# Optimization experiments

Hardware: AMD Instinct MI355X
Metric: run time of the kernel (lower is better)

The kernel has to match this reference:

```python
import jax, jax.numpy as jnp
import numpy as np

B, T, C, H = 2, 2048, 2048, 16
D = C // H  # 128


def _rope(x, cos, sin):
    # x: (B, T, H, D); cos/sin: (T, D//2) -> complex rotation on consecutive pairs
    xr = x.reshape(x.shape[0], x.shape[1], x.shape[2], D // 2, 2)
    x0, x1 = xr[..., 0], xr[..., 1]
    c = cos[None, :, None, :]
    s = sin[None, :, None, :]
    out = jnp.stack([x0 * c - x1 * s, x0 * s + x1 * c], axis=-1)
    return out.reshape(x.shape)


def setup_inputs() -> dict:
    key = jax.random.key(0)
    k1, k2, k3 = jax.random.split(key, 3)
    x = jax.random.normal(k1, (B, T, C), dtype=jnp.float32)
    w_qkv = jax.random.normal(k2, (3 * C, C), dtype=jnp.float32) * (C ** -0.5)
    w_proj = jax.random.normal(k3, (C, C), dtype=jnp.float32) * (C ** -0.5)
    # standard RoPE frequencies: theta_i = 10000^{-2i/D}
    inv_freq = 1.0 / (10000.0 ** (np.arange(0, D, 2, dtype=np.float32) / D))
    ang = np.outer(np.arange(T, dtype=np.float32), inv_freq)  # (T, D//2)
    freqs_cos = jnp.asarray(np.cos(ang), dtype=jnp.float32)
    freqs_sin = jnp.asarray(np.sin(ang), dtype=jnp.float32)
    return {"x": x, "w_qkv": w_qkv, "w_proj": w_proj,
            "freqs_cos": freqs_cos, "freqs_sin": freqs_sin}


def reference(x, w_qkv, w_proj, freqs_cos, freqs_sin):
    b, t, c = x.shape
    qkv = (x @ w_qkv.T).reshape(b, t, 3, H, D)
    q, k, v = qkv[:, :, 0], qkv[:, :, 1], qkv[:, :, 2]  # (B,T,H,D)
    q = _rope(q, freqs_cos, freqs_sin)
    k = _rope(k, freqs_cos, freqs_sin)
    scale = 1.0 / jnp.sqrt(jnp.float32(D))
    scores = jnp.einsum('bqhd,bkhd->bhqk', q, k) * scale  # (B,H,T,T)
    causal = jnp.tril(jnp.ones((t, t), dtype=bool))
    scores = jnp.where(causal[None, None], scores, jnp.finfo(scores.dtype).min)
    attn = jax.nn.softmax(scores, axis=-1)
    out = jnp.einsum('bhqk,bkhd->bqhd', attn, v).reshape(b, t, c)
    return out @ w_proj.T
```

## Files before the change

kernel.cpp:

```cpp
#include <hip/hip_runtime.h>
#include <hip/hip_bf16.h>

typedef float f32x4 __attribute__((ext_vector_type(4)));
typedef __bf16 bf16x8 __attribute__((ext_vector_type(8)));
typedef __bf16 bf16x4 __attribute__((ext_vector_type(4)));

constexpr int B_ = 2, T_ = 2048, C_ = 2048, H_ = 16, D_ = 128;
constexpr int M_ = B_ * T_;
constexpr int NQKV_ = 3 * C_;

__device__ __forceinline__ void gload_lds16(const void* g, void* l) {
    __builtin_amdgcn_global_load_lds(
        (const __attribute__((address_space(1))) unsigned int*)g,
        (__attribute__((address_space(3))) unsigned int*)l,
        16, 0, 0);
}

__global__ void cvt_kernel(const float* __restrict__ in, __bf16* __restrict__ out, int n4) {
    int i = blockIdx.x * blockDim.x + threadIdx.x;
    int stride = gridDim.x * blockDim.x;
    for (; i < n4; i += stride) {
        float4 v = reinterpret_cast<const float4*>(in)[i];
        bf16x4 o;
        o[0] = (__bf16)v.x; o[1] = (__bf16)v.y; o[2] = (__bf16)v.z; o[3] = (__bf16)v.w;
        reinterpret_cast<bf16x4*>(out)[i] = o;
    }
}

template <typename OutT>
__global__ __launch_bounds__(256, 3) void gemm_bt(
    const __bf16* __restrict__ A, const __bf16* __restrict__ Bm,
    OutT* __restrict__ Cm, int Mdim, int Ndim, int Kdim)
{
    __shared__ __align__(16) __bf16 As[128 * 64];
    __shared__ __align__(16) __bf16 Bs[128 * 64];
    const int tid = threadIdx.x;
    const int wave = tid >> 6, lane = tid & 63;
    const int fr = lane & 15, fq = lane >> 4;
    const int nbx = Ndim >> 7;
    const int bm = (blockIdx.x / nbx) << 7;
    const int bn = (blockIdx.x % nbx) << 7;
    const int wr = (wave >> 1) * 64, wc = (wave & 1) * 64;
    f32x4 acc[4][4] = {};
    const int srow = (wave << 5) + (lane >> 3);
    const int sch = lane & 7;
    const __bf16* Ag = A + (size_t)(bm + srow) * Kdim + sch * 8;
    const __bf16* Bg = Bm + (size_t)(bn + srow) * Kdim + sch * 8;

    for (int k0 = 0; k0 < Kdim; k0 += 64) {
        __syncthreads();
        #pragma unroll
        for (int p = 0; p < 4; ++p) {
            gload_lds16(Ag + (size_t)(8 * p) * Kdim + k0, (char*)As + (wave * 32 + 8 * p) * 128);
            gload_lds16(Bg + (size_t)(8 * p) * Kdim + k0, (char*)Bs + (wave * 32 + 8 * p) * 128);
        }
        __syncthreads();
        #pragma unroll
        for (int s = 0; s < 2; ++s) {
            bf16x8 af[4], bg[4];
            #pragma unroll
            for (int m = 0; m < 4; ++m)
                af[m] = *reinterpret_cast<const bf16x8*>((const char*)As + (wr + m * 16 + fr) * 128 + s * 64 + fq * 16);
            #pragma unroll
            for (int n = 0; n < 4; ++n)
                bg[n] = *reinterpret_cast<const bf16x8*>((const char*)Bs + (wc + n * 16 + fr) * 128 + s * 64 + fq * 16);
            #pragma unroll
            for (int m = 0; m < 4; ++m)
                #pragma unroll
                for (int n = 0; n < 4; ++n)
                    acc[m][n] = __builtin_amdgcn_mfma_f32_16x16x32_bf16(af[m], bg[n], acc[m][n], 0, 0, 0);
        }
    }
    #pragma unroll
    for (int m = 0; m < 4; ++m) {
        #pragma unroll
        for (int n = 0; n < 4; ++n) {
            int row0 = bm + wr + m * 16 + fq * 4;
            int col = bn + wc + n * 16 + fr;
            #pragma unroll
            for (int i = 0; i < 4; ++i)
                Cm[(size_t)(row0 + i) * Ndim + col] = (OutT)acc[m][n][i];
        }
    }
}

__global__ void rope_pack(const __bf16* __restrict__ qkv,
                          const float* __restrict__ fcos, const float* __restrict__ fsin,
                          __bf16* __restrict__ Q, __bf16* __restrict__ K, __bf16* __restrict__ V)
{
    const int row = blockIdx.x;
    const int b = row >> 11, t = row & (T_ - 1);
    const int tid = threadIdx.x;
    const int h = tid >> 4;
    const int jq = tid & 15;
    const float4 c4 = *reinterpret_cast<const float4*>(fcos + t * 64 + jq * 4);
    const float4 s4 = *reinterpret_cast<const float4*>(fsin + t * 64 + jq * 4);
    const float cc[4] = {c4.x, c4.y, c4.z, c4.w};
    const float ss[4] = {s4.x, s4.y, s4.z, s4.w};
    const __bf16* src = qkv + (size_t)row * NQKV_ + h * D_ + jq * 8;
    const size_t doff = ((size_t)(b * H_ + h) * T_ + t) * D_ + jq * 8;
    #pragma unroll
    for (int s = 0; s < 3; ++s) {
        bf16x8 v = *reinterpret_cast<const bf16x8*>(src + s * C_);
        bf16x8 o;
        if (s == 2) {
            o = v;
        } else {
            #pragma unroll
            for (int e = 0; e < 4; ++e) {
                float x0 = (float)v[2 * e], x1 = (float)v[2 * e + 1];
                o[2 * e]     = (__bf16)(x0 * cc[e] - x1 * ss[e]);
                o[2 * e + 1] = (__bf16)(x0 * ss[e] + x1 * cc[e]);
            }
        }
        __bf16* dst = (s == 0) ? Q : ((s == 1) ? K : V);
        *reinterpret_cast<bf16x8*>(dst + doff) = o;
    }
}

__global__ void transpose_v(const __bf16* __restrict__ V, __bf16* __restrict__ Vt) {
    const int bid = blockIdx.x;
    const int per_bh = (T_ / 64) * (D_ / 64);
    const int bh = bid / per_bh;
    const int rem = bid % per_bh;
    const int t0 = (rem / (D_ / 64)) * 64;
    const int d0 = (rem % (D_ / 64)) * 64;
    __shared__ __align__(16) __bf16 tile[64][72];
    const int tid = threadIdx.x;
    #pragma unroll
    for (int pass = 0; pass < 2; ++pass) {
        int r = pass * 32 + (tid >> 3);
        int ch = tid & 7;
        *reinterpret_cast<bf16x8*>(&tile[r][ch * 8]) =
            *reinterpret_cast<const bf16x8*>(V + ((size_t)bh * T_ + t0 + r) * D_ + d0 + ch * 8);
    }
    __syncthreads();
    #pragma unroll
    for (int pass = 0; pass < 2; ++pass) {
        int dr = pass * 32 + (tid >> 3);
        int ch = tid & 7;
        bf16x8 v;
        #pragma unroll
        for (int e = 0; e < 8; ++e) v[e] = tile[ch * 8 + e][dr];
        *reinterpret_cast<bf16x8*>(Vt + ((size_t)bh * D_ + d0 + dr) * T_ + t0 + ch * 8) = v;
    }
}

__global__ __launch_bounds__(256, 2) void attn_fwd(
    const __bf16* __restrict__ Q, const __bf16* __restrict__ K,
    const __bf16* __restrict__ Vt, __bf16* __restrict__ Out)
{
    const int bh = blockIdx.x;
    const int qt = (T_ / 128 - 1) - blockIdx.y;
    const int tid = threadIdx.x;
    const int wave = tid >> 6, lane = tid & 63;
    const int fr = lane & 15, fq = lane >> 4;
    __shared__ __align__(16) __bf16 Ks[64 * 128];
    __shared__ __align__(16) __bf16 Vs[128 * 64];
    __shared__ __align__(16) __bf16 Ps[4][32 * 64];

    const int q0 = qt * 128 + wave * 32;
    bf16x8 qf[2][4];
    #pragma unroll
    for (int m = 0; m < 2; ++m)
        #pragma unroll
        for (int ks = 0; ks < 4; ++ks)
            qf[m][ks] = *reinterpret_cast<const bf16x8*>(
                Q + ((size_t)bh * T_ + q0 + m * 16 + fr) * D_ + ks * 32 + 8 * fq);

    f32x4 oacc[2][8] = {};
    float mrow[2] = {-3.0e38f, -3.0e38f}, lrow[2] = {0.f, 0.f};
    const float scale = 0.08838834764831845f;
    char* pb = (char*)&Ps[wave][0];
    const int qmax = q0 + 31;
    const int ktmax = 2 * qt + 1;
    const int kr = lane >> 4, kch = lane & 15;
    const int vr = lane >> 3, vch = lane & 7;

    for (int kt = 0; kt <= ktmax; ++kt) {
        __syncthreads();
        #pragma unroll
        for (int p = 0; p < 4; ++p) {
            int row = 16 * wave + 4 * p + kr;
            gload_lds16(K + ((size_t)bh * T_ + kt * 64 + row) * D_ + ((kch ^ (row & 7)) << 3),
                        (char*)Ks + (16 * wave + 4 * p) * 256);
        }
        #pragma unroll
        for (int p = 0; p < 4; ++p) {
            int row = 32 * wave + 8 * p + vr;
            gload_lds16(Vt + ((size_t)bh * D_ + row) * T_ + kt * 64 + ((vch ^ (row & 7)) << 3),
                        (char*)Vs + (32 * wave + 8 * p) * 128);
        }
        __syncthreads();
        if (kt * 64 > qmax) continue;

        f32x4 sacc[2][4] = {};
        __builtin_amdgcn_s_setprio(1);
        #pragma unroll
        for (int ks = 0; ks < 4; ++ks) {
            #pragma unroll
            for (int f = 0; f < 4; ++f) {
                int row = f * 16 + fr;
                bf16x8 kf = *reinterpret_cast<const bf16x8*>(
                    (const char*)Ks + row * 256 + (((ks * 4 + fq) ^ (fr & 7)) << 4));
                sacc[0][f] = __builtin_amdgcn_mfma_f32_16x16x32_bf16(kf, qf[0][ks], sacc[0][f], 0, 0, 0);
                sacc[1][f] = __builtin_amdgcn_mfma_f32_16x16x32_bf16(kf, qf[1][ks], sacc[1][f], 0, 0, 0);
            }
        }
        __builtin_amdgcn_s_setprio(0);

        const bool diag = (kt >= 2 * qt);
        #pragma unroll
        for (int m = 0; m < 2; ++m) {
            const int qg = q0 + m * 16 + fr;
            const int r = m * 16 + fr;
            float mx = -3.0e38f;
            #pragma unroll
            for (int f = 0; f < 4; ++f)
                #pragma unroll
                for (int i = 0; i < 4; ++i) {
                    float sv = sacc[m][f][i] * scale;
                    if (diag && (kt * 64 + f * 16 + fq * 4 + i) > qg) sv = -3.0e38f;
                    sacc[m][f][i] = sv;
                    mx = fmaxf(mx, sv);
                }
            mx = fmaxf(mx, __shfl_xor(mx, 16, 64));
            mx = fmaxf(mx, __shfl_xor(mx, 32, 64));
            float mn = fmaxf(mrow[m], mx);
            float al = __expf(mrow[m] - mn);
            mrow[m] = mn;
            float rs = 0.f;
            #pragma unroll
            for (int f = 0; f < 4; ++f) {
                bf16x4 pv;
                #pragma unroll
                for (int i = 0; i < 4; ++i) {
                    float p = __expf(sacc[m][f][i] - mn);
                    rs += p;
                    pv[i] = (__bf16)p;
                }
                *reinterpret_cast<bf16x4*>(pb + r * 128 + ((f * 32 + fq * 8) ^ ((fr & 7) << 4))) = pv;
            }
            rs += __shfl_xor(rs, 16, 64);
            rs += __shfl_xor(rs, 32, 64);
            lrow[m] = lrow[m] * al + rs;
            float av[4];
            #pragma unroll
            for (int i = 0; i < 4; ++i) av[i] = __shfl(al, fq * 4 + i, 16);
            #pragma unroll
            for (int n = 0; n < 8; ++n)
                #pragma unroll
                for (int i = 0; i < 4; ++i) oacc[m][n][i] *= av[i];
        }

        __builtin_amdgcn_s_setprio(1);
        #pragma unroll
        for (int ks = 0; ks < 2; ++ks) {
            bf16x8 pa[2];
            #pragma unroll
            for (int m = 0; m < 2; ++m) {
                int r = m * 16 + fr;
                pa[m] = *reinterpret_cast<const bf16x8*>(pb + r * 128 + ((ks * 64 + fq * 16) ^ ((fr & 7) << 4)));
            }
            #pragma unroll
            for (int n = 0; n < 8; ++n) {
                int d = n * 16 + fr;
                bf16x8 vf = *reinterpret_cast<const bf16x8*>(
                    (const char*)Vs + d * 128 + (((ks * 4 + fq) ^ (fr & 7)) << 4));
                oacc[0][n] = __builtin_amdgcn_mfma_f32_16x16x32_bf16(pa[0], vf, oacc[0][n], 0, 0, 0);
                oacc[1][n] = __builtin_amdgcn_mfma_f32_16x16x32_bf16(pa[1], vf, oacc[1][n], 0, 0, 0);
            }
        }
        __builtin_amdgcn_s_setprio(0);
    }

    const int b = bh >> 4, h = bh & 15;
    #pragma unroll
    for (int m = 0; m < 2; ++m) {
        float linv[4];
        #pragma unroll
        for (int i = 0; i < 4; ++i) linv[i] = 1.0f / __shfl(lrow[m], fq * 4 + i, 16);
        #pragma unroll
        for (int n = 0; n < 8; ++n) {
            int d = n * 16 + fr;
            #pragma unroll
            for (int i = 0; i < 4; ++i) {
                int tg = qt * 128 + wave * 32 + m * 16 + fq * 4 + i;
                Out[((size_t)b * T_ + tg) * C_ + h * D_ + d] = (__bf16)(oacc[m][n][i] * linv[i]);
            }
        }
    }
}

extern "C" void kernel_launch(void* const* d_in, const int* in_sizes, int n_in,
                              void* d_out, int out_size, void* d_ws, size_t ws_size,
                              hipStream_t stream) {
    const float* x = (const float*)d_in[0];
    const float* w_qkv = (const float*)d_in[1];
    const float* w_proj = (const float*)d_in[2];
    const float* fcos = (const float*)d_in[3];
    const float* fsin = (const float*)d_in[4];
    float* out = (float*)d_out;

    char* ws = (char*)d_ws;
    size_t o = 0;
    __bf16* xb     = (__bf16*)(ws + o); o += (size_t)M_ * C_ * 2;
    __bf16* wqkvb  = (__bf16*)(ws + o); o += (size_t)NQKV_ * C_ * 2;
    __bf16* wprojb = (__bf16*)(ws + o); o += (size_t)C_ * C_ * 2;
    __bf16* qkvb   = (__bf16*)(ws + o); o += (size_t)M_ * NQKV_ * 2;
    __bf16* Qb     = (__bf16*)(ws + o); o += (size_t)M_ * C_ * 2;
    __bf16* Kb     = (__bf16*)(ws + o); o += (size_t)M_ * C_ * 2;
    __bf16* Vb     = wqkvb;
    __bf16* Vtb    = xb;
    __bf16* attnb  = qkvb;

    cvt_kernel<<<2048, 256, 0, stream>>>(x, xb, M_ * C_ / 4);
    cvt_kernel<<<2048, 256, 0, stream>>>(w_qkv, wqkvb, NQKV_ * C_ / 4);
    cvt_kernel<<<2048, 256, 0, stream>>>(w_proj, wprojb, C_ * C_ / 4);
    gemm_bt<__bf16><<<(M_ / 128) * (NQKV_ / 128), 256, 0, stream>>>(xb, wqkvb, qkvb, M_, NQKV_, C_);
    rope_pack<<<M_, 256, 0, stream>>>(qkvb, fcos, fsin, Qb, Kb, Vb);
    transpose_v<<<B_ * H_ * (T_ / 64) * (D_ / 64), 256, 0, stream>>>(Vb, Vtb);
    attn_fwd<<<dim3(B_ * H_, T_ / 128), 256, 0, stream>>>(Qb, Kb, Vtb, attnb);
    gemm_bt<float><<<(M_ / 128) * (C_ / 128), 256, 0, stream>>>(attnb, wprojb, out, M_, C_, C_);
}
```

Measured before the change: 409.3 us.

## Replace GEMM with 8-wave double-buffered pipelined kernel using swizzled LDS

Replaces the simple single-buffered 128x128 bf16 GEMM with an 8-wave, 256-column-tile kernel. Global-to-LDS loads are double-buffered and interleaved with MFMA phases under explicit barriers and waitcnts. LDS columns are XOR-swizzled to avoid bank conflicts, blocks are remapped across XCDs, and setprio is raised around the MFMAs. The aim is to hide memory latency and raise MFMA utilization in the QKV and output projections, at the cost of more LDS per block, more register pressure, and fragile hand-written synchronization.

```diff
diff --git a/kernel.cpp b/kernel.cpp
--- a/kernel.cpp
+++ b/kernel.cpp
@@ -27,56 +27,111 @@
     }
 }
 
-template <typename OutT>
-__global__ __launch_bounds__(256, 3) void gemm_bt(
-    const __bf16* __restrict__ A, const __bf16* __restrict__ Bm,
+
+#define PHASE(bs, q, dowait, ...) do {                                                         \
+    const char* Ab = Asb + (bs) * ABYTES;                                                      \
+    const char* Bb = Bsb + (bs) * 32768;                                                       \
+    bf16x8 af[QM][2];                                                                          \
+    _Pragma("unroll") for (int mj = 0; mj < QM; ++mj) {                                        \
+        int row = wrow + ((q) * QM + mj) * 16 + fr;                                            \
+        _Pragma("unroll") for (int ks = 0; ks < 2; ++ks)                                       \
+            af[mj][ks] = *reinterpret_cast<const bf16x8*>(                                     \
+                Ab + row * 128 + (((ks * 4 + fq) ^ (row & 7)) << 4));                          \
+    }                                                                                          \
+    if ((q) == 0) {                                                                            \
+        _Pragma("unroll") for (int n = 0; n < 4; ++n) {                                        \
+            int row = wcol + n * 16 + fr;                                                      \
+            _Pragma("unroll") for (int ks = 0; ks < 2; ++ks)                                   \
+                bg[n][ks] = *reinterpret_cast<const bf16x8*>(                                  \
+                    Bb + row * 128 + (((ks * 4 + fq) ^ (row & 7)) << 4));                      \
+        }                                                                                      \
+    }                                                                                          \
+    __VA_ARGS__;                                                                               \
+    __builtin_amdgcn_sched_barrier(0);                                                         \
+    __builtin_amdgcn_s_barrier();                                                              \
+    asm volatile("s_waitcnt lgkmcnt(0)" ::: "memory");                                         \
+    __builtin_amdgcn_sched_barrier(0);                                                         \
+    __builtin_amdgcn_s_setprio(1);                                                             \
+    _Pragma("unroll") for (int mj = 0; mj < QM; ++mj)                                          \
+        _Pragma("unroll") for (int n = 0; n < 4; ++n)                                          \
+            _Pragma("unroll") for (int ks = 0; ks < 2; ++ks)                                   \
+                acc[(q) * QM + mj][n] = __builtin_amdgcn_mfma_f32_16x16x32_bf16(               \
+                    af[mj][ks], bg[n][ks], acc[(q) * QM + mj][n], 0, 0, 0);                    \
+    __builtin_amdgcn_s_setprio(0);                                                             \
+    if (dowait) { asm volatile("s_waitcnt vmcnt(4)" ::: "memory"); }                           \
+    __builtin_amdgcn_sched_barrier(0);                                                         \
+    __builtin_amdgcn_s_barrier();                                                              \
+} while (0)
+
+template <int BM, typename OutT>
+__global__ __launch_bounds__(512, 2) void gemm8p(
+    const __bf16* __restrict__ A, const __bf16* __restrict__ Bmat,
     OutT* __restrict__ Cm, int Mdim, int Ndim, int Kdim)
 {
-    __shared__ __align__(16) __bf16 As[128 * 64];
-    __shared__ __align__(16) __bf16 Bs[128 * 64];
+    constexpr int MFR = BM / 32;
+    constexpr int QM  = MFR / 4;
+    constexpr int ABYTES = BM * 64 * 2;
+    __shared__ __align__(16) char Asb[2 * ABYTES];
+    __shared__ __align__(16) char Bsb[2 * 32768];
     const int tid = threadIdx.x;
-    const int wave = tid >> 6, lane = tid & 63;
+    const int w = tid >> 6, lane = tid & 63;
     const int fr = lane & 15, fq = lane >> 4;
-    const int nbx = Ndim >> 7;
-    const int bm = (blockIdx.x / nbx) << 7;
-    const int bn = (blockIdx.x % nbx) << 7;
-    const int wr = (wave >> 1) * 64, wc = (wave & 1) * 64;
-    f32x4 acc[4][4] = {};
-    const int srow = (wave << 5) + (lane >> 3);
-    const int sch = lane & 7;
-    const __bf16* Ag = A + (size_t)(bm + srow) * Kdim + sch * 8;
-    const __bf16* Bg = Bm + (size_t)(bn + srow) * Kdim + sch * 8;
-
-    for (int k0 = 0; k0 < Kdim; k0 += 64) {
-        __syncthreads();
-        #pragma unroll
-        for (int p = 0; p < 4; ++p) {
-            gload_lds16(Ag + (size_t)(8 * p) * Kdim + k0, (char*)As + (wave * 32 + 8 * p) * 128);
-            gload_lds16(Bg + (size_t)(8 * p) * Kdim + k0, (char*)Bs + (wave * 32 + 8 * p) * 128);
-        }
-        __syncthreads();
-        #pragma unroll
-        for (int s = 0; s < 2; ++s) {
-            bf16x8 af[4], bg[4];
-            #pragma unroll
-            for (int m = 0; m < 4; ++m)
-                af[m] = *reinterpret_cast<const bf16x8*>((const char*)As + (wr + m * 16 + fr) * 128 + s * 64 + fq * 16);
-            #pragma unroll
-            for (int n = 0; n < 4; ++n)
-                bg[n] = *reinterpret_cast<const bf16x8*>((const char*)Bs + (wc + n * 16 + fr) * 128 + s * 64 + fq * 16);
-            #pragma unroll
-            for (int m = 0; m < 4; ++m)
-                #pragma unroll
-                for (int n = 0; n < 4; ++n)
-                    acc[m][n] = __builtin_amdgcn_mfma_f32_16x16x32_bf16(af[m], bg[n], acc[m][n], 0, 0, 0);
-        }
-    }
-    #pragma unroll
-    for (int m = 0; m < 4; ++m) {
+    const int wm = w >> 2, wn = w & 3;
+    const int wrow = wm * (BM / 2), wcol = wn * 64;
+    const int NT = Kdim >> 6;
+    const int NIT = Kdim >> 7;
+    const int nbx = Ndim >> 8;
+    const int nwg = gridDim.x;
+    int bid = (blockIdx.x & 7) * (nwg >> 3) + (blockIdx.x >> 3);
+    const int bm = (bid / nbx) * BM;
+    const int bn = (bid % nbx) << 8;
+    const int srow8 = lane >> 3;
+    const int scol = ((lane & 7) ^ srow8) << 3;
+    const int dst2k = w * 2048;
+
+    f32x4 acc[MFR][4] = {};
+    bf16x8 bg[4][2];
+
+    auto stageB = [&](int db, int h, int t) {
+        int tt = t < NT ? t : NT - 1;
+        const __bf16* s0 = Bmat + (size_t)(bn + h * 128 + w * 16 + srow8) * Kdim + tt * 64 + scol;
+        char* d = Bsb + db * 32768 + h * 16384 + dst2k;
+        gload_lds16(s0, d);
+        gload_lds16(s0 + (size_t)8 * Kdim, d + 1024);
+    };
+    auto stageA = [&](int db, int h, int t) {
+        if (BM == 128 && h == 1) return;
+        int tt = t < NT ? t : NT - 1;
+        const __bf16* s0 = A + (size_t)(bm + h * 128 + w * 16 + srow8) * Kdim + tt * 64 + scol;
+        char* d = Asb + db * ABYTES + h * 16384 + dst2k;
+        gload_lds16(s0, d);
+        gload_lds16(s0 + (size_t)8 * Kdim, d + 1024);
+    };
+
+    stageB(0, 0, 0); stageB(0, 1, 0); stageA(0, 0, 0); stageA(0, 1, 0);
+    stageB(1, 0, 1); stageB(1, 1, 1);
+    asm volatile("s_waitcnt vmcnt(4)" ::: "memory");
+    __builtin_amdgcn_sched_barrier(0);
+    __builtin_amdgcn_s_barrier();
+
+    for (int it = 0; it < NIT; ++it) {
+        int t1 = 2 * it + 1, t2 = 2 * it + 2, t3 = 2 * it + 3;
+        PHASE(0, 0, 0, stageA(1, 0, t1));
+        PHASE(0, 1, 0, stageA(1, 1, t1); stageB(0, 0, t2));
+        PHASE(0, 2, 0, stageB(0, 1, t2));
+        PHASE(0, 3, 1, );
+        PHASE(1, 0, 0, stageA(0, 0, t2));
+        PHASE(1, 1, 0, stageA(0, 1, t2));
+        PHASE(1, 2, 0, stageB(1, 0, t3));
+        PHASE(1, 3, 1, stageB(1, 1, t3));
+    }
+
+    #pragma unroll
+    for (int m = 0; m < MFR; ++m) {
         #pragma unroll
         for (int n = 0; n < 4; ++n) {
-            int row0 = bm + wr + m * 16 + fq * 4;
-            int col = bn + wc + n * 16 + fr;
+            int row0 = bm + wrow + m * 16 + fq * 4;
+            int col = bn + wcol + n * 16 + fr;
             #pragma unroll
             for (int i = 0; i < 4; ++i)
                 Cm[(size_t)(row0 + i) * Ndim + col] = (OutT)acc[m][n][i];
@@ -317,9 +372,9 @@
     cvt_kernel<<<2048, 256, 0, stream>>>(x, xb, M_ * C_ / 4);
     cvt_kernel<<<2048, 256, 0, stream>>>(w_qkv, wqkvb, NQKV_ * C_ / 4);
     cvt_kernel<<<2048, 256, 0, stream>>>(w_proj, wprojb, C_ * C_ / 4);
-    gemm_bt<__bf16><<<(M_ / 128) * (NQKV_ / 128), 256, 0, stream>>>(xb, wqkvb, qkvb, M_, NQKV_, C_);
+    gemm8p<256, __bf16><<<(M_ / 256) * (NQKV_ / 256), 512, 0, stream>>>(xb, wqkvb, qkvb, M_, NQKV_, C_);
     rope_pack<<<M_, 256, 0, stream>>>(qkvb, fcos, fsin, Qb, Kb, Vb);
     transpose_v<<<B_ * H_ * (T_ / 64) * (D_ / 64), 256, 0, stream>>>(Vb, Vtb);
     attn_fwd<<<dim3(B_ * H_, T_ / 128), 256, 0, stream>>>(Qb, Kb, Vtb, attnb);
-    gemm_bt<float><<<(M_ / 128) * (C_ / 128), 256, 0, stream>>>(attnb, wprojb, out, M_, C_, C_);
-}
+    gemm8p<128, float><<<(M_ / 128) * (C_ / 256), 512, 0, stream>>>(attnb, wprojb, out, M_, C_, C_);
+}
```

Result: no change. 411.1 us (+0.4%).
